# Optimization experiments

Measured on AMD Instinct MI355X. Metric: run time of the kernel, lower is better.

The kernel has to match this reference:

```python
import jax, jax.numpy as jnp
import numpy as np

# Fully-refined octree (branching=2, initial_levels=7) == dense grid of resolution 128.
R = 128            # voxel grid resolution per axis (2**initial_levels)
SH_DIM = 9         # (sh_degree+1)**2, sh_degree=2
DATA_DIM = 28      # 3*SH_DIM + 1 (RGB SH coeffs + density)
N_STEPS = 128      # fixed ray-march step count (render_opt.n_steps)
BG = 1.0           # background brightness


def sh_basis(d):
    """Real SH basis up to degree 2 for unit directions d: [N,3] -> [N,9]."""
    x, y, z = d[:, 0], d[:, 1], d[:, 2]
    C0 = 0.28209479177387814
    C1 = 0.4886025119029199
    C2 = (1.0925484305920792, -1.0925484305920792, 0.31539156525252005,
          -1.0925484305920792, 0.5462742152960396)
    return jnp.stack([
        jnp.full_like(x, C0),
        -C1 * y, C1 * z, -C1 * x,
        C2[0] * x * y, C2[1] * y * z,
        C2[2] * (2.0 * z * z - x * x - y * y),
        C2[3] * x * z, C2[4] * (x * x - y * y),
    ], axis=-1)


def trilerp(grid, pts):
    """Trilinear interpolation. grid [R,R,R,C], pts [N,3] in grid coords."""
    Rg = grid.shape[0]
    p = jnp.clip(pts, 0.0, Rg - 1.0 - 1e-4)
    p0 = jnp.floor(p).astype(jnp.int32)
    w = p - p0.astype(p.dtype)
    out = jnp.zeros((pts.shape[0], grid.shape[-1]), grid.dtype)
    for dx in (0, 1):
        wx = w[:, 0] if dx else 1.0 - w[:, 0]
        for dy in (0, 1):
            wy = w[:, 1] if dy else 1.0 - w[:, 1]
            for dz in (0, 1):
                wz = w[:, 2] if dz else 1.0 - w[:, 2]
                out = out + (wx * wy * wz)[:, None] * grid[p0[:, 0] + dx, p0[:, 1] + dy, p0[:, 2] + dz]
    return out


def _render(grid, rays_o, rays_d, scaling, offset):
    dirs = rays_d / jnp.linalg.norm(rays_d, axis=-1, keepdims=True)   # world viewdirs
    o = rays_o * scaling + offset                                      # tree coords in [0,1]^3
    d = dirs * scaling
    delta_scale = 1.0 / jnp.linalg.norm(d, axis=-1)                    # world-space step scale
    invd = 1.0 / jnp.where(jnp.abs(d) > 1e-9, d, 1e-9)
    t1 = (0.0 - o) * invd
    t2 = (1.0 - o) * invd
    tmin = jnp.maximum(jnp.max(jnp.minimum(t1, t2), axis=-1), 0.0)
    tmax = jnp.min(jnp.maximum(t1, t2), axis=-1)
    valid = tmax > tmin
    dt = jnp.where(valid, (tmax - tmin) / N_STEPS, 0.0)                # per-ray step length
    basis = sh_basis(dirs)                                             # [N,9]
    N = rays_o.shape[0]

    def step(carry, i):
        T, rgb = carry
        t = tmin + (i.astype(grid.dtype) + 0.5) * dt
        pos = o + t[:, None] * d                                       # [N,3] in [0,1]^3
        vals = trilerp(grid, pos * R - 0.5)                            # [N,28]
        sigma = jnp.where(valid, jax.nn.relu(vals[:, -1]), 0.0)
        coeffs = vals[:, :3 * SH_DIM].reshape(N, 3, SH_DIM)
        c = jax.nn.sigmoid(jnp.einsum('nj,ncj->nc', basis, coeffs))    # [N,3]
        alpha = 1.0 - jnp.exp(-sigma * dt * delta_scale)
        rgb = rgb + (T * alpha)[:, None] * c
        T = T * (1.0 - alpha)
        return (T, rgb), None

    init = (jnp.ones((N,), grid.dtype), jnp.zeros((N, 3), grid.dtype))
    (T, rgb), _ = jax.lax.scan(step, init, jnp.arange(N_STEPS))
    return rgb + T[:, None] * BG


def setup_inputs() -> dict:
    key = jax.random.key(0)
    k1, k2, k3 = jax.random.split(key, 3)
    N = 32768
    rays_o = jax.random.uniform(k1, (N, 3), jnp.float32)               # inside unit cube
    rays_d = jax.random.normal(k2, (N, 3), jnp.float32)
    grid = jax.random.normal(k3, (R, R, R, DATA_DIM), jnp.float32) * 0.1  # octree leaf data
    scaling = jnp.ones((3,), jnp.float32)                              # 0.5/radius, radius=0.5
    offset = jnp.zeros((3,), jnp.float32)                              # 0.5 - center*scaling
    return {"rays_o": rays_o, "rays_d": rays_d, "grid": grid,
            "scaling": scaling, "offset": offset}


def reference(rays_o, rays_d, grid, scaling, offset):
    return _render(grid, rays_o, rays_d, scaling, offset)
```

## Files before the change

kernel.cpp:

```cpp
#include <hip/hip_runtime.h>
#include <math.h>

#define RGRID 128
#define NSTEPS 128
#define DATA_DIM 28

__device__ __forceinline__ float fast_rcp(float x) { return __builtin_amdgcn_rcpf(x); }

__global__ __launch_bounds__(256) void render_kernel(
    const float* __restrict__ rays_o,
    const float* __restrict__ rays_d,
    const float* __restrict__ grid,
    const float* __restrict__ scaling,
    const float* __restrict__ offset,
    float* __restrict__ out, int N)
{
    int tid = blockIdx.x * blockDim.x + threadIdx.x;
    int ray = tid >> 6;
    int lane = tid & 63;
    int s = lane >> 3;
    int c = lane & 7;
    if (ray >= N) return;

    float ox = rays_o[ray * 3 + 0], oy = rays_o[ray * 3 + 1], oz = rays_o[ray * 3 + 2];
    float rdx = rays_d[ray * 3 + 0], rdy = rays_d[ray * 3 + 1], rdz = rays_d[ray * 3 + 2];
    float sx = scaling[0], sy = scaling[1], sz = scaling[2];
    float fx = offset[0], fy = offset[1], fz = offset[2];

    float dn = rsqrtf(rdx * rdx + rdy * rdy + rdz * rdz);
    float dirx = rdx * dn, diry = rdy * dn, dirz = rdz * dn;

    float o0 = ox * sx + fx, o1 = oy * sy + fy, o2 = oz * sz + fz;
    float d0 = dirx * sx, d1 = diry * sy, d2 = dirz * sz;
    float delta_scale = rsqrtf(d0 * d0 + d1 * d1 + d2 * d2);

    float a0 = fabsf(d0) > 1e-9f ? d0 : 1e-9f;
    float a1 = fabsf(d1) > 1e-9f ? d1 : 1e-9f;
    float a2 = fabsf(d2) > 1e-9f ? d2 : 1e-9f;
    float i0 = 1.0f / a0, i1 = 1.0f / a1, i2 = 1.0f / a2;

    float t1x = (0.0f - o0) * i0, t2x = (1.0f - o0) * i0;
    float t1y = (0.0f - o1) * i1, t2y = (1.0f - o1) * i1;
    float t1z = (0.0f - o2) * i2, t2z = (1.0f - o2) * i2;
    float tmin = fmaxf(fmaxf(fminf(t1x, t2x), fminf(t1y, t2y)), fminf(t1z, t2z));
    tmin = fmaxf(tmin, 0.0f);
    float tmax = fminf(fminf(fmaxf(t1x, t2x), fmaxf(t1y, t2y)), fmaxf(t1z, t2z));
    bool valid = tmax > tmin;
    float dt = valid ? (tmax - tmin) * (1.0f / NSTEPS) : 0.0f;
    float sig_scale = dt * delta_scale;

    const float C0 = 0.28209479177387814f;
    const float C1 = 0.4886025119029199f;
    float b0 = C0;
    float b1 = -C1 * diry;
    float b2 = C1 * dirz;
    float b3 = -C1 * dirx;
    float b4 = 1.0925484305920792f * dirx * diry;
    float b5 = -1.0925484305920792f * diry * dirz;
    float b6 = 0.31539156525252005f * (2.0f * dirz * dirz - dirx * dirx - diry * diry);
    float b7 = -1.0925484305920792f * dirx * dirz;
    float b8 = 0.5462742152960396f * (dirx * dirx - diry * diry);

    int cdx = (c >> 2) & 1, cdy = (c >> 1) & 1, cdz = c & 1;
    int laneoff = (cdx << 14) + (cdy << 7) + cdz;
    float fsx = cdx ? 1.0f : -1.0f, fbx = cdx ? 0.0f : 1.0f;
    float fsy = cdy ? 1.0f : -1.0f, fby = cdy ? 0.0f : 1.0f;
    float fsz = cdz ? 1.0f : -1.0f, fbz = cdz ? 0.0f : 1.0f;

    float T = 1.0f, accr = 0.0f, accg = 0.0f, accb = 0.0f;
    float soff = (float)s + 0.5f;

    for (int it = 0; it < NSTEPS / 8; it++) {
        float t = tmin + ((float)(it * 8) + soff) * dt;
        float px = o0 + t * d0, py = o1 + t * d1, pz = o2 + t * d2;

        float gx = px * (float)RGRID - 0.5f;
        float gy = py * (float)RGRID - 0.5f;
        float gz = pz * (float)RGRID - 0.5f;
        gx = fminf(fmaxf(gx, 0.0f), 126.9999f);
        gy = fminf(fmaxf(gy, 0.0f), 126.9999f);
        gz = fminf(fmaxf(gz, 0.0f), 126.9999f);

        float flx = floorf(gx), fly = floorf(gy), flz = floorf(gz);
        int ix = (int)flx, iy = (int)fly, iz = (int)flz;
        float wx = gx - flx, wy = gy - fly, wz = gz - flz;

        float wgt = (fsx * wx + fbx) * (fsy * wy + fby) * (fsz * wz + fbz);

        int vox = (ix << 14) + (iy << 7) + iz + laneoff;
        const float4* gp = (const float4*)(grid + (size_t)vox * DATA_DIM);
        float4 v0 = gp[0], v1 = gp[1], v2 = gp[2], v3 = gp[3], v4 = gp[4], v5 = gp[5], v6 = gp[6];

        float vr = b0 * v0.x + b1 * v0.y + b2 * v0.z + b3 * v0.w
                 + b4 * v1.x + b5 * v1.y + b6 * v1.z + b7 * v1.w + b8 * v2.x;
        float vg = b0 * v2.y + b1 * v2.z + b2 * v2.w
                 + b3 * v3.x + b4 * v3.y + b5 * v3.z + b6 * v3.w
                 + b7 * v4.x + b8 * v4.y;
        float vb = b0 * v4.z + b1 * v4.w
                 + b2 * v5.x + b3 * v5.y + b4 * v5.z + b5 * v5.w
                 + b6 * v6.x + b7 * v6.y + b8 * v6.z;
        float vs = v6.w;

        vr *= wgt; vg *= wgt; vb *= wgt; vs *= wgt;

        #pragma unroll
        for (int m = 1; m < 8; m <<= 1) {
            vr += __shfl_xor(vr, m);
            vg += __shfl_xor(vg, m);
            vb += __shfl_xor(vb, m);
            vs += __shfl_xor(vs, m);
        }

        float sigma = valid ? fmaxf(vs, 0.0f) : 0.0f;
        float alpha = 1.0f - __expf(-sigma * sig_scale);
        float av = 1.0f - alpha;
        float br = alpha * fast_rcp(1.0f + __expf(-vr));
        float bg = alpha * fast_rcp(1.0f + __expf(-vg));
        float bb = alpha * fast_rcp(1.0f + __expf(-vb));

        #pragma unroll
        for (int d = 8; d < 64; d <<= 1) {
            float pa  = __shfl_up(av, d);
            float pbr = __shfl_up(br, d);
            float pbg = __shfl_up(bg, d);
            float pbb = __shfl_up(bb, d);
            if (lane >= d) {
                br = pbr + pa * br;
                bg = pbg + pa * bg;
                bb = pbb + pa * bb;
                av = pa * av;
            }
        }

        float ca  = __shfl(av, 63);
        float cbr = __shfl(br, 63);
        float cbg = __shfl(bg, 63);
        float cbb = __shfl(bb, 63);
        accr += T * cbr;
        accg += T * cbg;
        accb += T * cbb;
        T *= ca;
    }

    if (lane == 0) {
        out[ray * 3 + 0] = accr + T * 1.0f;
        out[ray * 3 + 1] = accg + T * 1.0f;
        out[ray * 3 + 2] = accb + T * 1.0f;
    }
}

extern "C" void kernel_launch(void* const* d_in, const int* in_sizes, int n_in,
                              void* d_out, int out_size, void* d_ws, size_t ws_size,
                              hipStream_t stream) {
    const float* rays_o  = (const float*)d_in[0];
    const float* rays_d  = (const float*)d_in[1];
    const float* grid    = (const float*)d_in[2];
    const float* scaling = (const float*)d_in[3];
    const float* offset  = (const float*)d_in[4];
    float* out = (float*)d_out;
    int N = in_sizes[0] / 3;

    int threads = 256;
    long long total = (long long)N * 64;
    int blocks = (int)((total + threads - 1) / threads);
    render_kernel<<<blocks, threads, 0, stream>>>(rays_o, rays_d, grid, scaling, offset, out, N);
}
```

Before: 487.7 us.

## Give each lane both z-corners and 16 samples per wave iteration

Each lane now loads two z-adjacent voxels, which are contiguous in memory, and does the z interpolation itself. A wave therefore processes 16 samples per iteration with 4 corner lanes each, instead of 8 samples with 8 lanes. This halves the loop trip count, shortens the corner-reduction shuffles, and extends the transmittance prefix scan to 16 segments. The final broadcast shuffles are dropped, so the running accumulation only stays correct in lane 63, which writes the output. The trade-off is more registers per lane for the extra 7 float4 loads.

```diff
diff --git a/kernel.cpp b/kernel.cpp
--- a/kernel.cpp
+++ b/kernel.cpp
@@ -18,8 +18,8 @@
     int tid = blockIdx.x * blockDim.x + threadIdx.x;
     int ray = tid >> 6;
     int lane = tid & 63;
-    int s = lane >> 3;
-    int c = lane & 7;
+    int s = lane >> 2;
+    int c = lane & 3;
     if (ray >= N) return;
 
     float ox = rays_o[ray * 3 + 0], oy = rays_o[ray * 3 + 1], oz = rays_o[ray * 3 + 2];
@@ -61,17 +61,16 @@
     float b7 = -1.0925484305920792f * dirx * dirz;
     float b8 = 0.5462742152960396f * (dirx * dirx - diry * diry);
 
-    int cdx = (c >> 2) & 1, cdy = (c >> 1) & 1, cdz = c & 1;
-    int laneoff = (cdx << 14) + (cdy << 7) + cdz;
+    int cdx = (c >> 1) & 1, cdy = c & 1;
+    int laneoff = (cdx << 14) + (cdy << 7);
     float fsx = cdx ? 1.0f : -1.0f, fbx = cdx ? 0.0f : 1.0f;
     float fsy = cdy ? 1.0f : -1.0f, fby = cdy ? 0.0f : 1.0f;
-    float fsz = cdz ? 1.0f : -1.0f, fbz = cdz ? 0.0f : 1.0f;
 
     float T = 1.0f, accr = 0.0f, accg = 0.0f, accb = 0.0f;
     float soff = (float)s + 0.5f;
 
-    for (int it = 0; it < NSTEPS / 8; it++) {
-        float t = tmin + ((float)(it * 8) + soff) * dt;
+    for (int it = 0; it < NSTEPS / 16; it++) {
+        float t = tmin + ((float)(it * 16) + soff) * dt;
         float px = o0 + t * d0, py = o1 + t * d1, pz = o2 + t * d2;
 
         float gx = px * (float)RGRID - 0.5f;
@@ -85,33 +84,45 @@
         int ix = (int)flx, iy = (int)fly, iz = (int)flz;
         float wx = gx - flx, wy = gy - fly, wz = gz - flz;
 
-        float wgt = (fsx * wx + fbx) * (fsy * wy + fby) * (fsz * wz + fbz);
+        float wgt = (fsx * wx + fbx) * (fsy * wy + fby);
 
         int vox = (ix << 14) + (iy << 7) + iz + laneoff;
         const float4* gp = (const float4*)(grid + (size_t)vox * DATA_DIM);
         float4 v0 = gp[0], v1 = gp[1], v2 = gp[2], v3 = gp[3], v4 = gp[4], v5 = gp[5], v6 = gp[6];
+        float4 u0 = gp[7], u1 = gp[8], u2 = gp[9], u3 = gp[10], u4 = gp[11], u5 = gp[12], u6 = gp[13];
 
-        float vr = b0 * v0.x + b1 * v0.y + b2 * v0.z + b3 * v0.w
-                 + b4 * v1.x + b5 * v1.y + b6 * v1.z + b7 * v1.w + b8 * v2.x;
-        float vg = b0 * v2.y + b1 * v2.z + b2 * v2.w
-                 + b3 * v3.x + b4 * v3.y + b5 * v3.z + b6 * v3.w
-                 + b7 * v4.x + b8 * v4.y;
-        float vb = b0 * v4.z + b1 * v4.w
-                 + b2 * v5.x + b3 * v5.y + b4 * v5.z + b5 * v5.w
-                 + b6 * v6.x + b7 * v6.y + b8 * v6.z;
-        float vs = v6.w;
+        float vr0 = b0 * v0.x + b1 * v0.y + b2 * v0.z + b3 * v0.w
+                  + b4 * v1.x + b5 * v1.y + b6 * v1.z + b7 * v1.w + b8 * v2.x;
+        float vg0 = b0 * v2.y + b1 * v2.z + b2 * v2.w
+                  + b3 * v3.x + b4 * v3.y + b5 * v3.z + b6 * v3.w
+                  + b7 * v4.x + b8 * v4.y;
+        float vb0 = b0 * v4.z + b1 * v4.w
+                  + b2 * v5.x + b3 * v5.y + b4 * v5.z + b5 * v5.w
+                  + b6 * v6.x + b7 * v6.y + b8 * v6.z;
+        float vs0 = v6.w;
 
-        vr *= wgt; vg *= wgt; vb *= wgt; vs *= wgt;
+        float vr1 = b0 * u0.x + b1 * u0.y + b2 * u0.z + b3 * u0.w
+                  + b4 * u1.x + b5 * u1.y + b6 * u1.z + b7 * u1.w + b8 * u2.x;
+        float vg1 = b0 * u2.y + b1 * u2.z + b2 * u2.w
+                  + b3 * u3.x + b4 * u3.y + b5 * u3.z + b6 * u3.w
+                  + b7 * u4.x + b8 * u4.y;
+        float vb1 = b0 * u4.z + b1 * u4.w
+                  + b2 * u5.x + b3 * u5.y + b4 * u5.z + b5 * u5.w
+                  + b6 * u6.x + b7 * u6.y + b8 * u6.z;
+        float vs1 = u6.w;
 
-        #pragma unroll
-        for (int m = 1; m < 8; m <<= 1) {
-            vr += __shfl_xor(vr, m);
-            vg += __shfl_xor(vg, m);
-            vb += __shfl_xor(vb, m);
-            vs += __shfl_xor(vs, m);
-        }
+        float wz0 = 1.0f - wz;
+        float vr = (vr0 * wz0 + vr1 * wz) * wgt;
+        float vg = (vg0 * wz0 + vg1 * wz) * wgt;
+        float vb = (vb0 * wz0 + vb1 * wz) * wgt;
+        float vs = (vs0 * wz0 + vs1 * wz) * wgt;
 
-        float sigma = valid ? fmaxf(vs, 0.0f) : 0.0f;
+        vr += __shfl_xor(vr, 1); vg += __shfl_xor(vg, 1);
+        vb += __shfl_xor(vb, 1); vs += __shfl_xor(vs, 1);
+        vr += __shfl_xor(vr, 2); vg += __shfl_xor(vg, 2);
+        vb += __shfl_xor(vb, 2); vs += __shfl_xor(vs, 2);
+
+        float sigma = fmaxf(vs, 0.0f);
         float alpha = 1.0f - __expf(-sigma * sig_scale);
         float av = 1.0f - alpha;
         float br = alpha * fast_rcp(1.0f + __expf(-vr));
@@ -119,7 +130,7 @@
         float bb = alpha * fast_rcp(1.0f + __expf(-vb));
 
         #pragma unroll
-        for (int d = 8; d < 64; d <<= 1) {
+        for (int d = 4; d < 64; d <<= 1) {
             float pa  = __shfl_up(av, d);
             float pbr = __shfl_up(br, d);
             float pbg = __shfl_up(bg, d);
@@ -132,17 +143,13 @@
             }
         }
 
-        float ca  = __shfl(av, 63);
-        float cbr = __shfl(br, 63);
-        float cbg = __shfl(bg, 63);
-        float cbb = __shfl(bb, 63);
-        accr += T * cbr;
-        accg += T * cbg;
-        accb += T * cbb;
-        T *= ca;
+        accr += T * br;
+        accg += T * bg;
+        accb += T * bb;
+        T *= av;
     }
 
-    if (lane == 0) {
+    if (lane == 63) {
         out[ray * 3 + 0] = accr + T * 1.0f;
         out[ray * 3 + 1] = accg + T * 1.0f;
         out[ray * 3 + 2] = accb + T * 1.0f;
```

New measurement: 738.9 us. +51.5%, slower.

## Double-buffer grid loads across march iterations and drop per-step broadcast shuffles

Applied to the files above, without the earlier changes.

Restructures the ray-march loop so the gather loads for the next 8-step chunk are issued before the SH/compositing compute of the current chunk, using two register buffers. Also removes the lane-63 broadcast shuffles by letting each lane accumulate its own running transmittance and color, with lane 63 (holding the full scan result) writing the output. This aims to hide gather latency and cut shuffle overhead, at the cost of more live registers that may lower occupancy.

```diff
diff --git a/kernel.cpp b/kernel.cpp
--- a/kernel.cpp
+++ b/kernel.cpp
@@ -70,27 +70,22 @@
     float T = 1.0f, accr = 0.0f, accg = 0.0f, accb = 0.0f;
     float soff = (float)s + 0.5f;
 
-    for (int it = 0; it < NSTEPS / 8; it++) {
-        float t = tmin + ((float)(it * 8) + soff) * dt;
+    auto calc = [&](int base, const float4*& gp, float& wgt) {
+        float t = tmin + ((float)base + soff) * dt;
         float px = o0 + t * d0, py = o1 + t * d1, pz = o2 + t * d2;
-
-        float gx = px * (float)RGRID - 0.5f;
-        float gy = py * (float)RGRID - 0.5f;
-        float gz = pz * (float)RGRID - 0.5f;
-        gx = fminf(fmaxf(gx, 0.0f), 126.9999f);
-        gy = fminf(fmaxf(gy, 0.0f), 126.9999f);
-        gz = fminf(fmaxf(gz, 0.0f), 126.9999f);
-
+        float gx = fminf(fmaxf(px * (float)RGRID - 0.5f, 0.0f), 126.9999f);
+        float gy = fminf(fmaxf(py * (float)RGRID - 0.5f, 0.0f), 126.9999f);
+        float gz = fminf(fmaxf(pz * (float)RGRID - 0.5f, 0.0f), 126.9999f);
         float flx = floorf(gx), fly = floorf(gy), flz = floorf(gz);
         int ix = (int)flx, iy = (int)fly, iz = (int)flz;
         float wx = gx - flx, wy = gy - fly, wz = gz - flz;
+        wgt = (fsx * wx + fbx) * (fsy * wy + fby) * (fsz * wz + fbz);
+        int vox = (ix << 14) + (iy << 7) + iz + laneoff;
+        gp = (const float4*)(grid + (size_t)vox * DATA_DIM);
+    };
 
-        float wgt = (fsx * wx + fbx) * (fsy * wy + fby) * (fsz * wz + fbz);
-
-        int vox = (ix << 14) + (iy << 7) + iz + laneoff;
-        const float4* gp = (const float4*)(grid + (size_t)vox * DATA_DIM);
-        float4 v0 = gp[0], v1 = gp[1], v2 = gp[2], v3 = gp[3], v4 = gp[4], v5 = gp[5], v6 = gp[6];
-
+    auto compute = [&](float4 v0, float4 v1, float4 v2, float4 v3,
+                       float4 v4, float4 v5, float4 v6, float wgt) {
         float vr = b0 * v0.x + b1 * v0.y + b2 * v0.z + b3 * v0.w
                  + b4 * v1.x + b5 * v1.y + b6 * v1.z + b7 * v1.w + b8 * v2.x;
         float vg = b0 * v2.y + b1 * v2.z + b2 * v2.w
@@ -132,17 +127,40 @@
             }
         }
 
-        float ca  = __shfl(av, 63);
-        float cbr = __shfl(br, 63);
-        float cbg = __shfl(bg, 63);
-        float cbb = __shfl(bb, 63);
-        accr += T * cbr;
-        accg += T * cbg;
-        accb += T * cbb;
-        T *= ca;
+        accr += T * br;
+        accg += T * bg;
+        accb += T * bb;
+        T *= av;
+    };
+
+    const float4 *gpA, *gpB;
+    float wA, wB;
+    float4 A0, A1, A2, A3, A4, A5, A6;
+    float4 B0, B1, B2, B3, B4, B5, B6;
+
+    calc(0, gpA, wA);
+    A0 = gpA[0]; A1 = gpA[1]; A2 = gpA[2]; A3 = gpA[3];
+    A4 = gpA[4]; A5 = gpA[5]; A6 = gpA[6];
+
+    for (int base = 0; base < NSTEPS - 16; base += 16) {
+        calc(base + 8, gpB, wB);
+        B0 = gpB[0]; B1 = gpB[1]; B2 = gpB[2]; B3 = gpB[3];
+        B4 = gpB[4]; B5 = gpB[5]; B6 = gpB[6];
+        compute(A0, A1, A2, A3, A4, A5, A6, wA);
+
+        calc(base + 16, gpA, wA);
+        A0 = gpA[0]; A1 = gpA[1]; A2 = gpA[2]; A3 = gpA[3];
+        A4 = gpA[4]; A5 = gpA[5]; A6 = gpA[6];
+        compute(B0, B1, B2, B3, B4, B5, B6, wB);
     }
 
-    if (lane == 0) {
+    calc(NSTEPS - 8, gpB, wB);
+    B0 = gpB[0]; B1 = gpB[1]; B2 = gpB[2]; B3 = gpB[3];
+    B4 = gpB[4]; B5 = gpB[5]; B6 = gpB[6];
+    compute(A0, A1, A2, A3, A4, A5, A6, wA);
+    compute(B0, B1, B2, B3, B4, B5, B6, wB);
+
+    if (lane == 63) {
         out[ray * 3 + 0] = accr + T * 1.0f;
         out[ray * 3 + 1] = accg + T * 1.0f;
         out[ray * 3 + 2] = accb + T * 1.0f;
```

New measurement: 502.7 us. 1.03x slower.
